# Kernel optimization log

Measured on AMD Instinct MI355X. Metric: run time of the kernel, lower is better.

Reference implementation:

```python
import jax, jax.numpy as jnp
import numpy as np

# dims
B = 4          # videos
F = 8          # frames (space_f)
P = 196        # patches per frame (time_n)
D = 768        # embed dim
H = 12         # heads
HD = D // H    # head dim
L = 4          # blocks
MLP = 4 * D
SCALE = HD ** -0.5
N = 1 + F * P  # sequence length with CLS


def setup_inputs() -> dict:
    key = jax.random.key(0)
    ks = jax.random.split(key, 20)
    s = 0.02
    w = lambda k, shape: (jax.random.normal(k, shape, jnp.float32) * s)
    inp = {
        'x': jax.random.normal(ks[0], (B, N, D), jnp.float32),
        # time attention params (stacked over layers); qkv_bias=False
        'qkv_w_t': w(ks[1], (L, 3 * D, D)),
        'proj_w_t': w(ks[2], (L, D, D)),
        'proj_b_t': jnp.zeros((L, D), jnp.float32),
        # space attention params
        'qkv_w_s': w(ks[3], (L, 3 * D, D)),
        'proj_w_s': w(ks[4], (L, D, D)),
        'proj_b_s': jnp.zeros((L, D), jnp.float32),
        # mlp
        'fc1_w': w(ks[5], (L, MLP, D)),
        'fc1_b': jnp.zeros((L, MLP), jnp.float32),
        'fc2_w': w(ks[6], (L, D, MLP)),
        'fc2_b': jnp.zeros((L, D), jnp.float32),
        # layernorms
        'ln1_g': jnp.ones((L, D), jnp.float32), 'ln1_b': jnp.zeros((L, D), jnp.float32),
        'ln2_g': jnp.ones((L, D), jnp.float32), 'ln2_b': jnp.zeros((L, D), jnp.float32),
        'ln3_g': jnp.ones((L, D), jnp.float32), 'ln3_b': jnp.zeros((L, D), jnp.float32),
    }
    return inp


def _ln(x, g, b):
    m = jnp.mean(x, axis=-1, keepdims=True)
    v = jnp.var(x, axis=-1, keepdims=True)
    return (x - m) * jax.lax.rsqrt(v + 1e-5) * g + b


def _attn(q, k, v):
    sim = jnp.einsum('bid,bjd->bij', q, k)
    a = jax.nn.softmax(sim, axis=-1)
    return jnp.einsum('bij,bjd->bid', a, v)


def _var_attn(x, qkv_w, proj_w, proj_b, mode):
    # x: [B, N, D]; mode in {'space','time'}
    qkv = x @ qkv_w.T                       # [B, N, 3D]
    q, k, v = jnp.split(qkv, 3, axis=-1)
    heads = lambda t: t.reshape(B, N, H, HD).transpose(0, 2, 1, 3).reshape(B * H, N, HD)
    q = heads(q) * SCALE
    k = heads(k)
    v = heads(v)
    cls_q, q_ = q[:, :1], q[:, 1:]
    cls_k, k_ = k[:, :1], k[:, 1:]
    cls_v, v_ = v[:, :1], v[:, 1:]
    # cls token attends over full sequence
    cls_out = _attn(cls_q, k, v)            # [(B h), 1, HD]
    BH = B * H
    if mode == 'space':
        # 'b (f n) d -> (b f) n d'
        split = lambda t: t.reshape(BH * F, P, HD)
        r, g, inner = F, F, P
    else:
        # 'b (f n) d -> (b n) f d'
        split = lambda t: t.reshape(BH, F, P, HD).transpose(0, 2, 1, 3).reshape(BH * P, F, HD)
        r, g, inner = P, P, F
    q_, k_, v_ = split(q_), split(k_), split(v_)
    # broadcast cls k/v across grouped batches: 'b () d -> (b r) () d'
    cls_k_r = jnp.repeat(cls_k, r, axis=0)
    cls_v_r = jnp.repeat(cls_v, r, axis=0)
    k_ = jnp.concatenate([cls_k_r, k_], axis=1)
    v_ = jnp.concatenate([cls_v_r, v_], axis=1)
    out = _attn(q_, k_, v_)                 # [(BH g), inner, HD]
    if mode == 'space':
        out = out.reshape(BH, F * P, HD)
    else:
        out = out.reshape(BH, P, F, HD).transpose(0, 2, 1, 3).reshape(BH, F * P, HD)
    out = jnp.concatenate([cls_out, out], axis=1)          # [(B h), N, HD]
    out = out.reshape(B, H, N, HD).transpose(0, 2, 1, 3).reshape(B, N, D)
    return out @ proj_w.T + proj_b


def _block(x, p):
    a = _ln(x, p['ln3_g'], p['ln3_b'])
    time_out = _var_attn(a, p['qkv_w_t'], p['proj_w_t'], p['proj_b_t'], 'time')
    time_residual = x + time_out
    space_out = _var_attn(_ln(time_residual, p['ln1_g'], p['ln1_b']),
                          p['qkv_w_s'], p['proj_w_s'], p['proj_b_s'], 'space')
    space_residual = x + space_out          # note: residual from original x (frozen-in-time style)
    h = _ln(space_residual, p['ln2_g'], p['ln2_b'])
    h = jax.nn.gelu(h @ p['fc1_w'].T + p['fc1_b'], approximate=False)
    h = h @ p['fc2_w'].T + p['fc2_b']
    return space_residual + h


def reference(x, qkv_w_t, proj_w_t, proj_b_t, qkv_w_s, proj_w_s, proj_b_s,
              fc1_w, fc1_b, fc2_w, fc2_b,
              ln1_g, ln1_b, ln2_g, ln2_b, ln3_g, ln3_b):
    params = dict(qkv_w_t=qkv_w_t, proj_w_t=proj_w_t, proj_b_t=proj_b_t,
                  qkv_w_s=qkv_w_s, proj_w_s=proj_w_s, proj_b_s=proj_b_s,
                  fc1_w=fc1_w, fc1_b=fc1_b, fc2_w=fc2_w, fc2_b=fc2_b,
                  ln1_g=ln1_g, ln1_b=ln1_b, ln2_g=ln2_g, ln2_b=ln2_b,
                  ln3_g=ln3_g, ln3_b=ln3_b)
    def step(carry, layer):
        return _block(carry, layer), None
    out, _ = jax.lax.scan(step, x, params)
    return out
```

## Files before the change

### kernel.cpp

```cpp
#include <hip/hip_runtime.h>
#include <cmath>

#define B_ 4
#define F_ 8
#define P_ 196
#define D_ 768
#define H_ 12
#define HD_ 64
#define L_ 4
#define MLP_ 3072
#define N_ (1 + F_*P_)
#define BN_ (B_*N_)
#define SCALE_ 0.125f
#define QKVC_ (3*D_)

typedef __bf16 bf16x8 __attribute__((ext_vector_type(8)));
typedef float f32x4 __attribute__((ext_vector_type(4)));
typedef const __attribute__((address_space(1))) void* gas_ptr;
typedef __attribute__((address_space(3))) void* las_ptr;

__device__ __forceinline__ unsigned short f2bf(float f) {
  union { __bf16 b; unsigned short u; } cv;
  cv.b = (__bf16)f;
  return cv.u;
}
__device__ __forceinline__ float bf2f(unsigned short u) {
  union { float f; unsigned int i; } cv; cv.i = ((unsigned int)u) << 16; return cv.f;
}
__device__ __forceinline__ unsigned int pk2(float a, float b) {
  return (unsigned int)f2bf(a) | ((unsigned int)f2bf(b) << 16);
}

__device__ __forceinline__ float gelu_exact(float x) {
  return 0.5f * x * (1.0f + erff(x * 0.70710678118654752f));
}

#define SQKV 1769472
#define SPROJ 589824
#define SFC 2359296

__device__ __forceinline__ void cvt_seg(const float* __restrict__ src,
                                        unsigned short* __restrict__ dst,
                                        int n, int t0, int stride) {
  for (int i = t0; i < (n >> 2); i += stride) {
    float4 v = ((const float4*)src)[i];
    ushort4 o;
    o.x = f2bf(v.x); o.y = f2bf(v.y); o.z = f2bf(v.z); o.w = f2bf(v.w);
    ((ushort4*)dst)[i] = o;
  }
}

__global__ __launch_bounds__(256) void cvt_layer_kernel(const float* qt, const float* pt,
                                                        const float* qs, const float* ps,
                                                        const float* f1, const float* f2,
                                                        unsigned short* wb) {
  int t0 = blockIdx.x * blockDim.x + threadIdx.x;
  int stride = gridDim.x * blockDim.x;
  cvt_seg(qt, wb + 0,       SQKV,  t0, stride);
  cvt_seg(pt, wb + 1769472, SPROJ, t0, stride);
  cvt_seg(qs, wb + 2359296, SQKV,  t0, stride);
  cvt_seg(ps, wb + 4128768, SPROJ, t0, stride);
  cvt_seg(f1, wb + 4718592, SFC,   t0, stride);
  cvt_seg(f2, wb + 7077888, SFC,   t0, stride);
}

__global__ __launch_bounds__(256) void ln_kernel(const float* __restrict__ x,
                                                 const float* __restrict__ g,
                                                 const float* __restrict__ b,
                                                 unsigned short* __restrict__ out) {
  int row = blockIdx.x;
  const float* xr = x + (size_t)row * D_;
  unsigned short* orow = out + (size_t)row * D_;
  int tid = threadIdx.x;
  float v0 = xr[tid], v1 = xr[tid + 256], v2 = xr[tid + 512];
  float s  = v0 + v1 + v2;
  float ss = v0*v0 + v1*v1 + v2*v2;
  #pragma unroll
  for (int o = 32; o > 0; o >>= 1) { s += __shfl_xor(s, o); ss += __shfl_xor(ss, o); }
  __shared__ float sm[8];
  int w = tid >> 6;
  if ((tid & 63) == 0) { sm[w*2] = s; sm[w*2+1] = ss; }
  __syncthreads();
  float tot  = sm[0] + sm[2] + sm[4] + sm[6];
  float tot2 = sm[1] + sm[3] + sm[5] + sm[7];
  float mean = tot * (1.0f/D_);
  float var  = tot2 * (1.0f/D_) - mean*mean;
  float rs   = rsqrtf(var + 1e-5f);
  orow[tid]       = f2bf((v0 - mean)*rs*g[tid]       + b[tid]);
  orow[tid + 256] = f2bf((v1 - mean)*rs*g[tid + 256] + b[tid + 256]);
  orow[tid + 512] = f2bf((v2 - mean)*rs*g[tid + 512] + b[tid + 512]);
}

template<int EPI>
__global__ __launch_bounds__(256, 3) void mfma_gemmP(const unsigned short* __restrict__ A,
                                                     const unsigned short* __restrict__ W,
                                                     const float* __restrict__ bias,
                                                     const float* __restrict__ Res,
                                                     void* __restrict__ Cout,
                                                     int M, int NN, int K) {
  __shared__ __align__(16) unsigned short LdsRaw[2*3*128*32];
  unsigned short* LdsA = LdsRaw;
  unsigned short* LdsB = LdsRaw + 3*128*32;
  int tid = threadIdx.x;
  int w = tid >> 6, l = tid & 63;
  int fr = l & 15, fq = l >> 4;
  int wr = w >> 1, wc = w & 1;
  int gx = (M + 127) >> 7;
  int gy = (NN + 127) >> 7;

  int nwg = gridDim.x;
  int orig = blockIdx.x;
  int q8 = nwg >> 3, r8 = nwg & 7;
  int xcd = orig & 7, idx = orig >> 3;
  int wg = (xcd < r8 ? xcd*(q8+1) : r8*(q8+1) + (xcd-r8)*q8) + idx;
  const int GROUPM = 8;
  int npg = GROUPM * gy;
  int gid = wg / npg;
  int first_m = gid * GROUPM;
  int gsz = gx - first_m; if (gsz > GROUPM) gsz = GROUPM;
  int rem = wg - gid * npg;
  int pid_m = first_m + rem % gsz;
  int pid_n = rem / gsz;
  int m0 = pid_m * 128, n0 = pid_n * 128;

  const char* aSrc[2]; const char* bSrc[2];
  #pragma unroll
  for (int q = 0; q < 2; ++q) {
    int c = q*256 + tid;
    int row = c >> 2;
    int cb = ((c & 3) << 4) ^ (((row >> 1) & 3) << 4);
    int ra = m0 + row; if (ra >= M) ra = M - 1;
    aSrc[q] = (const char*)A + ((size_t)ra * K) * 2 + cb;
    bSrc[q] = (const char*)W + ((size_t)(n0 + row) * K) * 2 + cb;
  }

  f32x4 acc[4][4] = {};
  int nt = K >> 5;
  int lswz = ((fr >> 1) & 3) << 4;

#define STAGEP(buf, kt) do { int kb_ = (kt) * 64;                                                                      \
    __builtin_amdgcn_global_load_lds((gas_ptr)(aSrc[0]+kb_), (las_ptr)(&LdsA[(buf)*4096 + (0*256 + w*64)*8]), 16, 0, 0); \
    __builtin_amdgcn_global_load_lds((gas_ptr)(aSrc[1]+kb_), (las_ptr)(&LdsA[(buf)*4096 + (1*256 + w*64)*8]), 16, 0, 0); \
    __builtin_amdgcn_global_load_lds((gas_ptr)(bSrc[0]+kb_), (las_ptr)(&LdsB[(buf)*4096 + (0*256 + w*64)*8]), 16, 0, 0); \
    __builtin_amdgcn_global_load_lds((gas_ptr)(bSrc[1]+kb_), (las_ptr)(&LdsB[(buf)*4096 + (1*256 + w*64)*8]), 16, 0, 0); \
  } while (0)

  STAGEP(0, 0);
  STAGEP(1, 1);
  int cur = 0;
  for (int t = 0; t < nt; ++t) {
    if (t + 1 < nt) {
      asm volatile("s_waitcnt vmcnt(4)" ::: "memory");
    } else {
      asm volatile("s_waitcnt vmcnt(0)" ::: "memory");
    }
    __builtin_amdgcn_s_barrier();
    const char* bufA = (const char*)(LdsA + cur*4096);
    const char* bufB = (const char*)(LdsB + cur*4096);
    bf16x8 afrag[4], bfrag[4];
    #pragma unroll
    for (int n = 0; n < 4; ++n)
      bfrag[n] = *(const bf16x8*)(bufB + (wc*64 + n*16 + fr)*64 + ((fq*16) ^ lswz));
    #pragma unroll
    for (int m = 0; m < 4; ++m)
      afrag[m] = *(const bf16x8*)(bufA + (wr*64 + m*16 + fr)*64 + ((fq*16) ^ lswz));
    #pragma unroll
    for (int m = 0; m < 4; ++m)
      #pragma unroll
      for (int n = 0; n < 4; ++n)
        acc[m][n] = __builtin_amdgcn_mfma_f32_16x16x32_bf16(afrag[m], bfrag[n], acc[m][n], 0, 0, 0);
    if (t + 2 < nt) {
      int nb = cur + 2; if (nb >= 3) nb -= 3;
      STAGEP(nb, t + 2);
    }
    ++cur; if (cur == 3) cur = 0;
  }
#undef STAGEP

  float* eps = (float*)LdsRaw;
  #pragma unroll
  for (int h = 0; h < 2; ++h) {
    __syncthreads();
    if (wr == h) {
      #pragma unroll
      for (int n = 0; n < 4; ++n)
        #pragma unroll
        for (int i = 0; i < 4; ++i)
          #pragma unroll
          for (int r = 0; r < 4; ++r) {
            int lrow = i*16 + fq*4 + r;
            int col  = wc*64 + n*16 + fr;
            eps[lrow*128 + (col ^ (((lrow >> 2) & 7) << 2))] = acc[i][n][r];
          }
    }
    __syncthreads();
    #pragma unroll
    for (int p = 0; p < 8; ++p) {
      int idx = p*256 + tid;
      int lrow = idx >> 5, cg = idx & 31;
      int col0 = cg * 4;
      int grow = m0 + h*64 + lrow;
      if (grow < M) {
        f32x4 v = *(const f32x4*)&eps[lrow*128 + (col0 ^ (((lrow >> 2) & 7) << 2))];
        int gcol = n0 + col0;
        if (EPI == 1 || EPI == 2) {
          float4 bv = *(const float4*)&bias[gcol];
          v[0] += bv.x; v[1] += bv.y; v[2] += bv.z; v[3] += bv.w;
        }
        if (EPI == 1) {
          float4 rv = *(const float4*)&Res[(size_t)grow * NN + gcol];
          v[0] += rv.x; v[1] += rv.y; v[2] += rv.z; v[3] += rv.w;
          *(float4*)&((float*)Cout)[(size_t)grow * NN + gcol] = make_float4(v[0], v[1], v[2], v[3]);
        } else if (EPI == 0) {
          *(float4*)&((float*)Cout)[(size_t)grow * NN + gcol] = make_float4(v[0], v[1], v[2], v[3]);
        } else {
          if (EPI == 2) {
            v[0] = gelu_exact(v[0]); v[1] = gelu_exact(v[1]);
            v[2] = gelu_exact(v[2]); v[3] = gelu_exact(v[3]);
          }
          unsigned long long ov = (unsigned long long)pk2(v[0], v[1])
                                | ((unsigned long long)pk2(v[2], v[3]) << 32);
          *(unsigned long long*)&((unsigned short*)Cout)[(size_t)grow * NN + gcol] = ov;
        }
      }
    }
  }
}

template<int EPI>
__global__ __launch_bounds__(256, 2) void mfma_gemmW(const unsigned short* __restrict__ A,
                                                     const unsigned short* __restrict__ W,
                                                     const float* __restrict__ bias,
                                                     const float* __restrict__ Res,
                                                     void* __restrict__ Cout,
                                                     int M, int NN, int K) {
  __shared__ __align__(16) unsigned short LdsRaw[3*256*32 + 3*128*32];
  unsigned short* LdsA = LdsRaw;
  unsigned short* LdsB = LdsRaw + 3*256*32;
  int tid = threadIdx.x;
  int w = tid >> 6, l = tid & 63;
  int fr = l & 15, fq = l >> 4;
  int wr = w >> 1, wc = w & 1;
  int gx = (M + 255) >> 8;
  int gy = (NN + 127) >> 7;

  int nwg = gridDim.x;
  int orig = blockIdx.x;
  int q8 = nwg >> 3, r8 = nwg & 7;
  int xcd = orig & 7, idx = orig >> 3;
  int wg = (xcd < r8 ? xcd*(q8+1) : r8*(q8+1) + (xcd-r8)*q8) + idx;
  const int GROUPM = 4;
  int npg = GROUPM * gy;
  int gid = wg / npg;
  int first_m = gid * GROUPM;
  int gsz = gx - first_m; if (gsz > GROUPM) gsz = GROUPM;
  int rem = wg - gid * npg;
  int pid_m = first_m + rem % gsz;
  int pid_n = rem / gsz;
  int m0 = pid_m * 256, n0 = pid_n * 128;

  const char* aSrc[4]; const char* bSrc[2];
  #pragma unroll
  for (int q = 0; q < 4; ++q) {
    int c = q*256 + tid;
    int row = c >> 2;
    int cb = ((c & 3) << 4) ^ (((row >> 1) & 3) << 4);
    int ra = m0 + row; if (ra >= M) ra = M - 1;
    aSrc[q] = (const char*)A + ((size_t)ra * K) * 2 + cb;
  }
  #pragma unroll
  for (int q = 0; q < 2; ++q) {
    int c = q*256 + tid;
    int row = c >> 2;
    int cb = ((c & 3) << 4) ^ (((row >> 1) & 3) << 4);
    bSrc[q] = (const char*)W + ((size_t)(n0 + row) * K) * 2 + cb;
  }

  f32x4 acc[8][4] = {};
  int nt = K >> 5;
  int lswz = ((fr >> 1) & 3) << 4;

#define STAGEW(buf, kt) do { int kb_ = (kt) * 64;                                                                      \
    __builtin_amdgcn_global_load_lds((gas_ptr)(aSrc[0]+kb_), (las_ptr)(&LdsA[(buf)*8192 + (0*256 + w*64)*8]), 16, 0, 0); \
    __builtin_amdgcn_global_load_lds((gas_ptr)(aSrc[1]+kb_), (las_ptr)(&LdsA[(buf)*8192 + (1*256 + w*64)*8]), 16, 0, 0); \
    __builtin_amdgcn_global_load_lds((gas_ptr)(aSrc[2]+kb_), (las_ptr)(&LdsA[(buf)*8192 + (2*256 + w*64)*8]), 16, 0, 0); \
    __builtin_amdgcn_global_load_lds((gas_ptr)(aSrc[3]+kb_), (las_ptr)(&LdsA[(buf)*8192 + (3*256 + w*64)*8]), 16, 0, 0); \
    __builtin_amdgcn_global_load_lds((gas_ptr)(bSrc[0]+kb_), (las_ptr)(&LdsB[(buf)*4096 + (0*256 + w*64)*8]), 16, 0, 0); \
    __builtin_amdgcn_global_load_lds((gas_ptr)(bSrc[1]+kb_), (las_ptr)(&LdsB[(buf)*4096 + (1*256 + w*64)*8]), 16, 0, 0); \
  } while (0)

  STAGEW(0, 0);
  STAGEW(1, 1);
  int cur = 0;
  for (int t = 0; t < nt; ++t) {
    if (t + 1 < nt) {
      asm volatile("s_waitcnt vmcnt(6)" ::: "memory");
    } else {
      asm volatile("s_waitcnt vmcnt(0)" ::: "memory");
    }
    __builtin_amdgcn_s_barrier();
    const char* bufA = (const char*)(LdsA + cur*8192);
    const char* bufB = (const char*)(LdsB + cur*4096);
    bf16x8 afrag[8], bfrag[4];
    #pragma unroll
    for (int n = 0; n < 4; ++n)
      bfrag[n] = *(const bf16x8*)(bufB + (wc*64 + n*16 + fr)*64 + ((fq*16) ^ lswz));
    #pragma unroll
    for (int m = 0; m < 8; ++m)
      afrag[m] = *(const bf16x8*)(bufA + (wr*128 + m*16 + fr)*64 + ((fq*16) ^ lswz));
    #pragma unroll
    for (int m = 0; m < 8; ++m)
      #pragma unroll
      for (int n = 0; n < 4; ++n)
        acc[m][n] = __builtin_amdgcn_mfma_f32_16x16x32_bf16(afrag[m], bfrag[n], acc[m][n], 0, 0, 0);
    if (t + 2 < nt) {
      int nb = cur + 2; if (nb >= 3) nb -= 3;
      STAGEW(nb, t + 2);
    }
    ++cur; if (cur == 3) cur = 0;
  }
#undef STAGEW

  float* eps = (float*)LdsRaw;
  #pragma unroll
  for (int qh = 0; qh < 4; ++qh) {
    __syncthreads();
    if (wr == (qh >> 1)) {
      int mbase = (qh & 1) * 4;
      #pragma unroll
      for (int n = 0; n < 4; ++n)
        #pragma unroll
        for (int mi = 0; mi < 4; ++mi)
          #pragma unroll
          for (int r = 0; r < 4; ++r) {
            int lrow = mi*16 + fq*4 + r;
            int col  = wc*64 + n*16 + fr;
            eps[lrow*128 + (col ^ (((lrow >> 2) & 7) << 2))] = acc[mbase + mi][n][r];
          }
    }
    __syncthreads();
    #pragma unroll
    for (int p = 0; p < 8; ++p) {
      int idx = p*256 + tid;
      int lrow = idx >> 5, cg = idx & 31;
      int col0 = cg * 4;
      int grow = m0 + qh*64 + lrow;
      if (grow < M) {
        f32x4 v = *(const f32x4*)&eps[lrow*128 + (col0 ^ (((lrow >> 2) & 7) << 2))];
        int gcol = n0 + col0;
        if (EPI == 1 || EPI == 2) {
          float4 bv = *(const float4*)&bias[gcol];
          v[0] += bv.x; v[1] += bv.y; v[2] += bv.z; v[3] += bv.w;
        }
        if (EPI == 1) {
          float4 rv = *(const float4*)&Res[(size_t)grow * NN + gcol];
          v[0] += rv.x; v[1] += rv.y; v[2] += rv.z; v[3] += rv.w;
          *(float4*)&((float*)Cout)[(size_t)grow * NN + gcol] = make_float4(v[0], v[1], v[2], v[3]);
        } else if (EPI == 0) {
          *(float4*)&((float*)Cout)[(size_t)grow * NN + gcol] = make_float4(v[0], v[1], v[2], v[3]);
        } else {
          if (EPI == 2) {
            v[0] = gelu_exact(v[0]); v[1] = gelu_exact(v[1]);
            v[2] = gelu_exact(v[2]); v[3] = gelu_exact(v[3]);
          }
          unsigned long long ov = (unsigned long long)pk2(v[0], v[1])
                                | ((unsigned long long)pk2(v[2], v[3]) << 32);
          *(unsigned long long*)&((unsigned short*)Cout)[(size_t)grow * NN + gcol] = ov;
        }
      }
    }
  }
}

#define CLS_CH 7
#define CLS_CHSZ 256
__global__ __launch_bounds__(256) void cls_attn_part(const unsigned short* __restrict__ qkv,
                                                     float* __restrict__ part) {
  int blk = blockIdx.x;
  int c = blk % CLS_CH, bh = blk / CLS_CH;
  int b = bh / H_, h = bh % H_;
  const unsigned short* base = qkv + (size_t)b * N_ * QKVC_ + h * HD_;
  __shared__ float q[HD_];
  __shared__ float s[CLS_CHSZ];
  __shared__ float redm[4], redd[4];
  __shared__ float pvs[4][HD_];
  int tid = threadIdx.x;
  if (tid < HD_) q[tid] = bf2f(base[tid]) * SCALE_;
  __syncthreads();
  int j = c * CLS_CHSZ + tid;
  float sc = -1e30f;
  if (j < N_) {
    const unsigned short* kp = base + (size_t)j * QKVC_ + D_;
    float acc = 0.f;
    #pragma unroll
    for (int cc = 0; cc < 8; ++cc) {
      uint4 kv = *(const uint4*)(kp + cc*8);
      const unsigned short* e = (const unsigned short*)&kv;
      #pragma unroll
      for (int t = 0; t < 8; ++t) acc = fmaf(q[cc*8+t], bf2f(e[t]), acc);
    }
    sc = acc;
  }
  float m = sc;
  #pragma unroll
  for (int o = 32; o > 0; o >>= 1) m = fmaxf(m, __shfl_xor(m, o));
  if ((tid & 63) == 0) redm[tid >> 6] = m;
  __syncthreads();
  m = fmaxf(fmaxf(redm[0], redm[1]), fmaxf(redm[2], redm[3]));
  float p = (j < N_) ? __expf(sc - m) : 0.f;
  s[tid] = p;
  float den = p;
  #pragma unroll
  for (int o = 32; o > 0; o >>= 1) den += __shfl_xor(den, o);
  if ((tid & 63) == 0) redd[tid >> 6] = den;
  __syncthreads();
  float dtot = redd[0] + redd[1] + redd[2] + redd[3];
  int lane = tid & 63, g = tid >> 6;
  float acc = 0.f;
  #pragma unroll 8
  for (int i = 0; i < CLS_CHSZ/4; ++i) {
    int jl = g + 4*i;
    int jj = c * CLS_CHSZ + jl;
    if (jj < N_) acc = fmaf(s[jl], bf2f(base[(size_t)jj * QKVC_ + 2*D_ + lane]), acc);
  }
  pvs[g][lane] = acc;
  __syncthreads();
  if (g == 0) {
    float pv = pvs[0][lane] + pvs[1][lane] + pvs[2][lane] + pvs[3][lane];
    float* pp = part + ((size_t)bh * CLS_CH + c) * 66;
    if (lane == 0) { pp[0] = m; pp[1] = dtot; }
    pp[2 + lane] = pv;
  }
}

__global__ __launch_bounds__(64) void cls_attn_reduce(const float* __restrict__ part,
                                                      unsigned short* __restrict__ att) {
  int bh = blockIdx.x;
  int b = bh / H_, h = bh % H_;
  int lane = threadIdx.x;
  const float* pp = part + (size_t)bh * CLS_CH * 66;
  float m = -1e30f;
  #pragma unroll
  for (int c = 0; c < CLS_CH; ++c) m = fmaxf(m, pp[c*66]);
  float den = 0.f, acc = 0.f;
  #pragma unroll
  for (int c = 0; c < CLS_CH; ++c) {
    float wfac = __expf(pp[c*66] - m);
    den += pp[c*66 + 1] * wfac;
    acc += pp[c*66 + 2 + lane] * wfac;
  }
  att[(size_t)(b * N_) * D_ + h * HD_ + lane] = f2bf(acc / den);
}

__global__ __launch_bounds__(256) void space_attn_mfma(const unsigned short* __restrict__ qkv,
                                                       unsigned short* __restrict__ att) {
  int blk = blockIdx.x;
  int f = blk % F_; int bh = blk / F_;
  int b = bh / H_, h = bh % H_;
  const unsigned short* qbase = qkv + (size_t)b * N_ * QKVC_ + h * HD_;
  __shared__ __align__(16) unsigned short Ksm[208*64];
  __shared__ __align__(16) unsigned short Vtm[64*256];
  __shared__ __align__(16) unsigned short Pm[4*16*256];
  int tid = threadIdx.x;

  for (int c = tid; c < 208*8; c += 256) {
    int j = c >> 3, cb = (c & 7) * 16;
    uint4 val = make_uint4(0,0,0,0);
    if (j < 197) {
      int n = (j == 0) ? 0 : (1 + f*P_ + j - 1);
      val = *(const uint4*)(qbase + (size_t)n*QKVC_ + D_ + cb/2);
    }
    *(uint4*)((char*)Ksm + j*128 + (cb ^ ((j&7)<<4))) = val;
  }
  for (int c = tid; c < 112*8; c += 256) {
    int jj = c % 112, dc = c / 112;
    int j0 = jj * 2;
    uint4 r0 = make_uint4(0,0,0,0), r1 = make_uint4(0,0,0,0);
    if (j0 < 197) {
      int n = (j0 == 0) ? 0 : (1 + f*P_ + j0 - 1);
      r0 = *(const uint4*)(qbase + (size_t)n*QKVC_ + 2*D_ + dc*8);
    }
    if (j0 + 1 < 197) {
      int n = 1 + f*P_ + j0;
      r1 = *(const uint4*)(qbase + (size_t)n*QKVC_ + 2*D_ + dc*8);
    }
    const unsigned short* e0 = (const unsigned short*)&r0;
    const unsigned short* e1 = (const unsigned short*)&r1;
    #pragma unroll
    for (int e = 0; e < 8; ++e) {
      int d = dc*8 + e;
      unsigned int pk = (unsigned int)e0[e] | ((unsigned int)e1[e] << 16);
      *(unsigned int*)((char*)Vtm + d*512 + ((2*j0) ^ ((d&7)<<4))) = pk;
    }
  }
  int w = tid >> 6, l = tid & 63;
  int fr = l & 15, fq = l >> 4;
  char* Pw = (char*)Pm + w * 8192;
  {
    int q = l >> 2, cb = 416 + (l & 3) * 8;
    *(unsigned long long*)(Pw + q*512 + (cb ^ ((q&7)<<4))) = 0ull;
  }
  __syncthreads();

  int swz = (fr & 7) << 4;
  for (int qt = w; qt <= 12; qt += 4) {
    int qrow = qt*16 + fr; if (qrow > 195) qrow = 195;
    int n_q = 1 + f*P_ + qrow;
    bf16x8 qf0 = *(const bf16x8*)(qbase + (size_t)n_q*QKVC_ + fq*8);
    bf16x8 qf1 = *(const bf16x8*)(qbase + (size_t)n_q*QKVC_ + 32 + fq*8);
    f32x4 s[13];
    #pragma unroll
    for (int jt = 0; jt < 13; ++jt) s[jt] = (f32x4){0.f,0.f,0.f,0.f};
    #pragma unroll
    for (int jt = 0; jt < 13; ++jt) {
      bf16x8 a0 = *(const bf16x8*)((char*)Ksm + (jt*16+fr)*128 + ((fq*16) ^ swz));
      s[jt] = __builtin_amdgcn_mfma_f32_16x16x32_bf16(a0, qf0, s[jt], 0, 0, 0);
      bf16x8 a1 = *(const bf16x8*)((char*)Ksm + (jt*16+fr)*128 + ((64 + fq*16) ^ swz));
      s[jt] = __builtin_amdgcn_mfma_f32_16x16x32_bf16(a1, qf1, s[jt], 0, 0, 0);
    }
    float m = -1e30f;
    #pragma unroll
    for (int jt = 0; jt < 13; ++jt) {
      #pragma unroll
      for (int r = 0; r < 4; ++r) {
        if (jt*16 + fq*4 + r < 197) m = fmaxf(m, s[jt][r]);
      }
    }
    m = fmaxf(m, __shfl_xor(m, 16));
    m = fmaxf(m, __shfl_xor(m, 32));
    float den = 0.f;
    #pragma unroll
    for (int jt = 0; jt < 13; ++jt) {
      #pragma unroll
      for (int r = 0; r < 4; ++r) {
        float p = (jt*16 + fq*4 + r < 197) ? __expf((s[jt][r] - m) * SCALE_) : 0.f;
        s[jt][r] = p;
        den += p;
      }
    }
    den += __shfl_xor(den, 16);
    den += __shfl_xor(den, 32);
    #pragma unroll
    for (int jt = 0; jt < 13; ++jt) {
      unsigned long long pv = (unsigned long long)pk2(s[jt][0], s[jt][1])
                            | ((unsigned long long)pk2(s[jt][2], s[jt][3]) << 32);
      *(unsigned long long*)(Pw + fr*512 + ((jt*32 + fq*8) ^ swz)) = pv;
    }
    float rden = 1.0f / den;
    bool wr_ok = (qt*16 + fr) < 196;
    int n_out = 1 + f*P_ + qt*16 + fr;
    #pragma unroll
    for (int dt = 0; dt < 4; ++dt) {
      f32x4 o = (f32x4){0.f,0.f,0.f,0.f};
      #pragma unroll
      for (int ks = 0; ks < 7; ++ks) {
        bf16x8 av = *(const bf16x8*)((char*)Vtm + (dt*16+fr)*512 + ((ks*64 + fq*16) ^ swz));
        bf16x8 bp = *(const bf16x8*)(Pw + fr*512 + ((ks*64 + fq*16) ^ swz));
        o = __builtin_amdgcn_mfma_f32_16x16x32_bf16(av, bp, o, 0, 0, 0);
      }
      if (wr_ok) {
        unsigned long long ov = (unsigned long long)pk2(o[0]*rden, o[1]*rden)
                              | ((unsigned long long)pk2(o[2]*rden, o[3]*rden) << 32);
        *(unsigned long long*)(att + (size_t)(b*N_ + n_out)*D_ + h*HD_ + dt*16 + fq*4) = ov;
      }
    }
  }
}

__global__ __launch_bounds__(256) void time_attn_kernel(const unsigned short* __restrict__ qkv,
                                                        unsigned short* __restrict__ att) {
  int idx = blockIdx.x * 4 + (threadIdx.x >> 6);
  int bh = idx / P_, p = idx % P_;
  int b = bh / H_, h = bh % H_;
  int lane = threadIdx.x & 63;
  const unsigned short* base = qkv + (size_t)b * N_ * QKVC_ + h * HD_ + lane;
  float k[9], v[9];
  k[0] = bf2f(base[D_]);
  v[0] = bf2f(base[2*D_]);
  #pragma unroll
  for (int j = 0; j < 8; ++j) {
    size_t r = (size_t)(1 + j * P_ + p) * QKVC_;
    k[j+1] = bf2f(base[r + D_]);
    v[j+1] = bf2f(base[r + 2*D_]);
  }
  #pragma unroll 1
  for (int f = 0; f < F_; ++f) {
    size_t qr = (size_t)(1 + f * P_ + p) * QKVC_;
    float qd = bf2f(base[qr]) * SCALE_;
    float s[9];
    #pragma unroll
    for (int j = 0; j < 9; ++j) {
      float prod = qd * k[j];
      #pragma unroll
      for (int o = 32; o > 0; o >>= 1) prod += __shfl_xor(prod, o);
      s[j] = prod;
    }
    float m = s[0];
    #pragma unroll
    for (int j = 1; j < 9; ++j) m = fmaxf(m, s[j]);
    float den = 0.f, o_ = 0.f;
    #pragma unroll
    for (int j = 0; j < 9; ++j) {
      float pj = __expf(s[j] - m);
      den += pj;
      o_ = fmaf(pj, v[j], o_);
    }
    att[(size_t)(b * N_ + 1 + f * P_ + p) * D_ + h * HD_ + lane] = f2bf(o_ / den);
  }
}

extern "C" void kernel_launch(void* const* d_in, const int* in_sizes, int n_in,
                              void* d_out, int out_size, void* d_ws, size_t ws_size,
                              hipStream_t stream) {
  const float* x_in     = (const float*)d_in[0];
  const float* qkv_w_t  = (const float*)d_in[1];
  const float* proj_w_t = (const float*)d_in[2];
  const float* proj_b_t = (const float*)d_in[3];
  const float* qkv_w_s  = (const float*)d_in[4];
  const float* proj_w_s = (const float*)d_in[5];
  const float* proj_b_s = (const float*)d_in[6];
  const float* fc1_w    = (const float*)d_in[7];
  const float* fc1_b    = (const float*)d_in[8];
  const float* fc2_w    = (const float*)d_in[9];
  const float* fc2_b    = (const float*)d_in[10];
  const float* ln1_g    = (const float*)d_in[11];
  const float* ln1_b    = (const float*)d_in[12];
  const float* ln2_g    = (const float*)d_in[13];
  const float* ln2_b    = (const float*)d_in[14];
  const float* ln3_g    = (const float*)d_in[15];
  const float* ln3_b    = (const float*)d_in[16];

  float* X_out = (float*)d_out;
  char* ws = (char*)d_ws;
  unsigned short* Wbf = (unsigned short*)ws;
  const size_t WOFF = 18874368;
  unsigned short* QKVbf = (unsigned short*)(ws + WOFF);
  unsigned short* Hbf   = (unsigned short*)(ws + WOFF);
  float*          TR    = (float*)(ws + WOFF + 57839616);
  unsigned short* Abf   = (unsigned short*)(ws + WOFF + 57839616 + 19279872);
  float*          CLSP  = (float*)(ws + WOFF + 57839616 + 19279872 + 9639936);

  unsigned short* wqkv_t = Wbf + 0;
  unsigned short* wproj_t= Wbf + 1769472;
  unsigned short* wqkv_s = Wbf + 2359296;
  unsigned short* wproj_s= Wbf + 4128768;
  unsigned short* wfc1   = Wbf + 4718592;
  unsigned short* wfc2   = Wbf + 7077888;

  dim3 blk(256);
  dim3 g_qkv(25 * 18), g_fc1(25 * 24);
  dim3 g_proj(50 * 6), g_fc2(50 * 6);

  for (int l = 0; l < L_; ++l) {
    const float* X = (l == 0) ? x_in : (const float*)X_out;
    cvt_layer_kernel<<<2048, blk, 0, stream>>>(
        qkv_w_t + (size_t)l*SQKV, proj_w_t + (size_t)l*SPROJ,
        qkv_w_s + (size_t)l*SQKV, proj_w_s + (size_t)l*SPROJ,
        fc1_w + (size_t)l*SFC, fc2_w + (size_t)l*SFC, Wbf);
    ln_kernel<<<BN_, blk, 0, stream>>>(X, ln3_g + l*D_, ln3_b + l*D_, Abf);
    mfma_gemmW<3><<<g_qkv, blk, 0, stream>>>(Abf, wqkv_t, nullptr, nullptr, QKVbf, BN_, QKVC_, D_);
    cls_attn_part<<<B_*H_*CLS_CH, blk, 0, stream>>>(QKVbf, CLSP);
    cls_attn_reduce<<<B_*H_, dim3(64), 0, stream>>>(CLSP, Abf);
    time_attn_kernel<<<(B_*H_*P_)/4, blk, 0, stream>>>(QKVbf, Abf);
    mfma_gemmP<1><<<g_proj, blk, 0, stream>>>(Abf, wproj_t, proj_b_t + l*D_, X, TR, BN_, D_, D_);
    ln_kernel<<<BN_, blk, 0, stream>>>(TR, ln1_g + l*D_, ln1_b + l*D_, Abf);
    mfma_gemmW<3><<<g_qkv, blk, 0, stream>>>(Abf, wqkv_s, nullptr, nullptr, QKVbf, BN_, QKVC_, D_);
    cls_attn_part<<<B_*H_*CLS_CH, blk, 0, stream>>>(QKVbf, CLSP);
    cls_attn_reduce<<<B_*H_, dim3(64), 0, stream>>>(CLSP, Abf);
    space_attn_mfma<<<B_*H_*F_, blk, 0, stream>>>(QKVbf, Abf);
    mfma_gemmP<1><<<g_proj, blk, 0, stream>>>(Abf, wproj_s, proj_b_s + l*D_, X, TR, BN_, D_, D_);
    ln_kernel<<<BN_, blk, 0, stream>>>(TR, ln2_g + l*D_, ln2_b + l*D_, Abf);
    mfma_gemmW<2><<<g_fc1, blk, 0, stream>>>(Abf, wfc1, fc1_b + l*MLP_, nullptr, Hbf, BN_, MLP_, D_);
    mfma_gemmP<1><<<g_fc2, blk, 0, stream>>>(Hbf, wfc2, fc2_b + l*D_, TR, X_out, BN_, D_, MLP_);
  }
}
```

Measured before the change: 1.832 ms.

## Shrink GEMM tiles, switch to double-buffered LDS, and retile N=768 GEMMs

The GEMM kernels move from triple-buffered LDS to double buffering, with an explicit LDS-read fence and barrier before the next stage overwrites the current buffer. The wide 256x128 kernel becomes a 128x64 kernel used for the N=768 projection and fc2 GEMMs, while QKV and fc1 now use the 128x128 kernel with occupancy raised to 4 blocks. The aim is higher occupancy and more workgroups on the smaller GEMMs, at the cost of less data reuse per tile, an extra barrier per k-step, and a shallower prefetch pipeline.

```diff
diff --git a/kernel.cpp b/kernel.cpp
--- a/kernel.cpp
+++ b/kernel.cpp
@@ -34,6 +34,11 @@
 __device__ __forceinline__ float gelu_exact(float x) {
   return 0.5f * x * (1.0f + erff(x * 0.70710678118654752f));
 }
+
+#define LDS_READ_FENCE() do {                                  \
+    asm volatile("s_waitcnt lgkmcnt(0)" ::: "memory");         \
+    __builtin_amdgcn_sched_barrier(0);                         \
+  } while (0)
 
 #define SQKV 1769472
 #define SPROJ 589824
@@ -92,15 +97,15 @@
 }
 
 template<int EPI>
-__global__ __launch_bounds__(256, 3) void mfma_gemmP(const unsigned short* __restrict__ A,
+__global__ __launch_bounds__(256, 4) void mfma_gemmP(const unsigned short* __restrict__ A,
                                                      const unsigned short* __restrict__ W,
                                                      const float* __restrict__ bias,
                                                      const float* __restrict__ Res,
                                                      void* __restrict__ Cout,
                                                      int M, int NN, int K) {
-  __shared__ __align__(16) unsigned short LdsRaw[2*3*128*32];
+  __shared__ __align__(16) unsigned short LdsRaw[2*2*128*32];
   unsigned short* LdsA = LdsRaw;
-  unsigned short* LdsB = LdsRaw + 3*128*32;
+  unsigned short* LdsB = LdsRaw + 2*128*32;
   int tid = threadIdx.x;
   int w = tid >> 6, l = tid & 63;
   int fr = l & 15, fq = l >> 4;
@@ -169,11 +174,12 @@
       #pragma unroll
       for (int n = 0; n < 4; ++n)
         acc[m][n] = __builtin_amdgcn_mfma_f32_16x16x32_bf16(afrag[m], bfrag[n], acc[m][n], 0, 0, 0);
+    LDS_READ_FENCE();
+    __builtin_amdgcn_s_barrier();
     if (t + 2 < nt) {
-      int nb = cur + 2; if (nb >= 3) nb -= 3;
-      STAGEP(nb, t + 2);
-    }
-    ++cur; if (cur == 3) cur = 0;
+      STAGEP(cur, t + 2);
+    }
+    cur ^= 1;
   }
 #undef STAGEP
 
@@ -228,28 +234,28 @@
 }
 
 template<int EPI>
-__global__ __launch_bounds__(256, 2) void mfma_gemmW(const unsigned short* __restrict__ A,
+__global__ __launch_bounds__(256, 4) void mfma_gemmN(const unsigned short* __restrict__ A,
                                                      const unsigned short* __restrict__ W,
                                                      const float* __restrict__ bias,
                                                      const float* __restrict__ Res,
                                                      void* __restrict__ Cout,
                                                      int M, int NN, int K) {
-  __shared__ __align__(16) unsigned short LdsRaw[3*256*32 + 3*128*32];
+  __shared__ __align__(16) unsigned short LdsRaw[2*128*32 + 2*64*32];
   unsigned short* LdsA = LdsRaw;
-  unsigned short* LdsB = LdsRaw + 3*256*32;
+  unsigned short* LdsB = LdsRaw + 2*128*32;
   int tid = threadIdx.x;
   int w = tid >> 6, l = tid & 63;
   int fr = l & 15, fq = l >> 4;
   int wr = w >> 1, wc = w & 1;
-  int gx = (M + 255) >> 8;
-  int gy = (NN + 127) >> 7;
+  int gx = (M + 127) >> 7;
+  int gy = (NN + 63) >> 6;
 
   int nwg = gridDim.x;
   int orig = blockIdx.x;
   int q8 = nwg >> 3, r8 = nwg & 7;
   int xcd = orig & 7, idx = orig >> 3;
   int wg = (xcd < r8 ? xcd*(q8+1) : r8*(q8+1) + (xcd-r8)*q8) + idx;
-  const int GROUPM = 4;
+  const int GROUPM = 8;
   int npg = GROUPM * gy;
   int gid = wg / npg;
   int first_m = gid * GROUPM;
@@ -257,96 +263,92 @@
   int rem = wg - gid * npg;
   int pid_m = first_m + rem % gsz;
   int pid_n = rem / gsz;
-  int m0 = pid_m * 256, n0 = pid_n * 128;
-
-  const char* aSrc[4]; const char* bSrc[2];
-  #pragma unroll
-  for (int q = 0; q < 4; ++q) {
+  int m0 = pid_m * 128, n0 = pid_n * 64;
+
+  const char* aSrc[2]; const char* bSrc;
+  #pragma unroll
+  for (int q = 0; q < 2; ++q) {
     int c = q*256 + tid;
     int row = c >> 2;
     int cb = ((c & 3) << 4) ^ (((row >> 1) & 3) << 4);
     int ra = m0 + row; if (ra >= M) ra = M - 1;
     aSrc[q] = (const char*)A + ((size_t)ra * K) * 2 + cb;
   }
-  #pragma unroll
-  for (int q = 0; q < 2; ++q) {
-    int c = q*256 + tid;
+  {
+    int c = tid;
     int row = c >> 2;
     int cb = ((c & 3) << 4) ^ (((row >> 1) & 3) << 4);
-    bSrc[q] = (const char*)W + ((size_t)(n0 + row) * K) * 2 + cb;
-  }
-
-  f32x4 acc[8][4] = {};
+    bSrc = (const char*)W + ((size_t)(n0 + row) * K) * 2 + cb;
+  }
+
+  f32x4 acc[4][2] = {};
   int nt = K >> 5;
   int lswz = ((fr >> 1) & 3) << 4;
 
-#define STAGEW(buf, kt) do { int kb_ = (kt) * 64;                                                                      \
-    __builtin_amdgcn_global_load_lds((gas_ptr)(aSrc[0]+kb_), (las_ptr)(&LdsA[(buf)*8192 + (0*256 + w*64)*8]), 16, 0, 0); \
-    __builtin_amdgcn_global_load_lds((gas_ptr)(aSrc[1]+kb_), (las_ptr)(&LdsA[(buf)*8192 + (1*256 + w*64)*8]), 16, 0, 0); \
-    __builtin_amdgcn_global_load_lds((gas_ptr)(aSrc[2]+kb_), (las_ptr)(&LdsA[(buf)*8192 + (2*256 + w*64)*8]), 16, 0, 0); \
-    __builtin_amdgcn_global_load_lds((gas_ptr)(aSrc[3]+kb_), (las_ptr)(&LdsA[(buf)*8192 + (3*256 + w*64)*8]), 16, 0, 0); \
-    __builtin_amdgcn_global_load_lds((gas_ptr)(bSrc[0]+kb_), (las_ptr)(&LdsB[(buf)*4096 + (0*256 + w*64)*8]), 16, 0, 0); \
-    __builtin_amdgcn_global_load_lds((gas_ptr)(bSrc[1]+kb_), (las_ptr)(&LdsB[(buf)*4096 + (1*256 + w*64)*8]), 16, 0, 0); \
+#define STAGEN(buf, kt) do { int kb_ = (kt) * 64;                                                                      \
+    __builtin_amdgcn_global_load_lds((gas_ptr)(aSrc[0]+kb_), (las_ptr)(&LdsA[(buf)*4096 + (0*256 + w*64)*8]), 16, 0, 0); \
+    __builtin_amdgcn_global_load_lds((gas_ptr)(aSrc[1]+kb_), (las_ptr)(&LdsA[(buf)*4096 + (1*256 + w*64)*8]), 16, 0, 0); \
+    __builtin_amdgcn_global_load_lds((gas_ptr)(bSrc+kb_),    (las_ptr)(&LdsB[(buf)*2048 + (w*64)*8]),         16, 0, 0); \
   } while (0)
 
-  STAGEW(0, 0);
-  STAGEW(1, 1);
+  STAGEN(0, 0);
+  STAGEN(1, 1);
   int cur = 0;
   for (int t = 0; t < nt; ++t) {
     if (t + 1 < nt) {
-      asm volatile("s_waitcnt vmcnt(6)" ::: "memory");
+      asm volatile("s_waitcnt vmcnt(3)" ::: "memory");
     } else {
       asm volatile("s_waitcnt vmcnt(0)" ::: "memory");
     }
     __builtin_amdgcn_s_barrier();
-    const char* bufA = (const char*)(LdsA + cur*8192);
-    const char* bufB = (const char*)(LdsB + cur*4096);
-    bf16x8 afrag[8], bfrag[4];
-    #pragma unroll
-    for (int n = 0; n < 4; ++n)
-      bfrag[n] = *(const bf16x8*)(bufB + (wc*64 + n*16 + fr)*64 + ((fq*16) ^ lswz));
-    #pragma unroll
-    for (int m = 0; m < 8; ++m)
-      afrag[m] = *(const bf16x8*)(bufA + (wr*128 + m*16 + fr)*64 + ((fq*16) ^ lswz));
-    #pragma unroll
-    for (int m = 0; m < 8; ++m)
-      #pragma unroll
-      for (int n = 0; n < 4; ++n)
+    const char* bufA = (const char*)(LdsA + cur*4096);
+    const char* bufB = (const char*)(LdsB + cur*2048);
+    bf16x8 afrag[4], bfrag[2];
+    #pragma unroll
+    for (int n = 0; n < 2; ++n)
+      bfrag[n] = *(const bf16x8*)(bufB + (wc*32 + n*16 + fr)*64 + ((fq*16) ^ lswz));
+    #pragma unroll
+    for (int m = 0; m < 4; ++m)
+      afrag[m] = *(const bf16x8*)(bufA + (wr*64 + m*16 + fr)*64 + ((fq*16) ^ lswz));
+    #pragma unroll
+    for (int m = 0; m < 4; ++m)
+      #pragma unroll
+      for (int n = 0; n < 2; ++n)
         acc[m][n] = __builtin_amdgcn_mfma_f32_16x16x32_bf16(afrag[m], bfrag[n], acc[m][n], 0, 0, 0);
+    LDS_READ_FENCE();
+    __builtin_amdgcn_s_barrier();
     if (t + 2 < nt) {
-      int nb = cur + 2; if (nb >= 3) nb -= 3;
-      STAGEW(nb, t + 2);
-    }
-    ++cur; if (cur == 3) cur = 0;
-  }
-#undef STAGEW
+      STAGEN(cur, t + 2);
+    }
+    cur ^= 1;
+  }
+#undef STAGEN
 
   float* eps = (float*)LdsRaw;
   #pragma unroll
-  for (int qh = 0; qh < 4; ++qh) {
+  for (int h = 0; h < 2; ++h) {
     __syncthreads();
-    if (wr == (qh >> 1)) {
-      int mbase = (qh & 1) * 4;
-      #pragma unroll
-      for (int n = 0; n < 4; ++n)
+    if (wr == h) {
+      #pragma unroll
+      for (int n = 0; n < 2; ++n)
         #pragma unroll
-        for (int mi = 0; mi < 4; ++mi)
+        for (int i = 0; i < 4; ++i)
           #pragma unroll
           for (int r = 0; r < 4; ++r) {
-            int lrow = mi*16 + fq*4 + r;
-            int col  = wc*64 + n*16 + fr;
-            eps[lrow*128 + (col ^ (((lrow >> 2) & 7) << 2))] = acc[mbase + mi][n][r];
+            int lrow = i*16 + fq*4 + r;
+            int col  = wc*32 + n*16 + fr;
+            eps[lrow*64 + (col ^ (((lrow >> 2) & 7) << 2))] = acc[i][n][r];
           }
     }
     __syncthreads();
     #pragma unroll
-    for (int p = 0; p < 8; ++p) {
+    for (int p = 0; p < 4; ++p) {
       int idx = p*256 + tid;
-      int lrow = idx >> 5, cg = idx & 31;
+      int lrow = idx >> 4, cg = idx & 15;
       int col0 = cg * 4;
-      int grow = m0 + qh*64 + lrow;
+      int grow = m0 + h*64 + lrow;
       if (grow < M) {
-        f32x4 v = *(const f32x4*)&eps[lrow*128 + (col0 ^ (((lrow >> 2) & 7) << 2))];
+        f32x4 v = *(const f32x4*)&eps[lrow*64 + (col0 ^ (((lrow >> 2) & 7) << 2))];
         int gcol = n0 + col0;
         if (EPI == 1 || EPI == 2) {
           float4 bv = *(const float4*)&bias[gcol];
@@ -648,8 +650,8 @@
   unsigned short* wfc2   = Wbf + 7077888;
 
   dim3 blk(256);
-  dim3 g_qkv(25 * 18), g_fc1(25 * 24);
-  dim3 g_proj(50 * 6), g_fc2(50 * 6);
+  dim3 g_qkv(50 * 18), g_fc1(50 * 24);
+  dim3 g_n768(50 * 12);
 
   for (int l = 0; l < L_; ++l) {
     const float* X = (l == 0) ? x_in : (const float*)X_out;
@@ -658,19 +660,19 @@
         qkv_w_s + (size_t)l*SQKV, proj_w_s + (size_t)l*SPROJ,
         fc1_w + (size_t)l*SFC, fc2_w + (size_t)l*SFC, Wbf);
     ln_kernel<<<BN_, blk, 0, stream>>>(X, ln3_g + l*D_, ln3_b + l*D_, Abf);
-    mfma_gemmW<3><<<g_qkv, blk, 0, stream>>>(Abf, wqkv_t, nullptr, nullptr, QKVbf, BN_, QKVC_, D_);
+    mfma_gemmP<3><<<g_qkv, blk, 0, stream>>>(Abf, wqkv_t, nullptr, nullptr, QKVbf, BN_, QKVC_, D_);
     cls_attn_part<<<B_*H_*CLS_CH, blk, 0, stream>>>(QKVbf, CLSP);
     cls_attn_reduce<<<B_*H_, dim3(64), 0, stream>>>(CLSP, Abf);
     time_attn_kernel<<<(B_*H_*P_)/4, blk, 0, stream>>>(QKVbf, Abf);
-    mfma_gemmP<1><<<g_proj, blk, 0, stream>>>(Abf, wproj_t, proj_b_t + l*D_, X, TR, BN_, D_, D_);
+    mfma_gemmN<1><<<g_n768, blk, 0, stream>>>(Abf, wproj_t, proj_b_t + l*D_, X, TR, BN_, D_, D_);
     ln_kernel<<<BN_, blk, 0, stream>>>(TR, ln1_g + l*D_, ln1_b + l*D_, Abf);
-    mfma_gemmW<3><<<g_qkv, blk, 0, stream>>>(Abf, wqkv_s, nullptr, nullptr, QKVbf, BN_, QKVC_, D_);
+    mfma_gemmP<3><<<g_qkv, blk, 0, stream>>>(Abf, wqkv_s, nullptr, nullptr, QKVbf, BN_, QKVC_, D_);
     cls_attn_part<<<B_*H_*CLS_CH, blk, 0, stream>>>(QKVbf, CLSP);
     cls_attn_reduce<<<B_*H_, dim3(64), 0, stream>>>(CLSP, Abf);
     space_attn_mfma<<<B_*H_*F_, blk, 0, stream>>>(QKVbf, Abf);
-    mfma_gemmP<1><<<g_proj, blk, 0, stream>>>(Abf, wproj_s, proj_b_s + l*D_, X, TR, BN_, D_, D_);
+    mfma_gemmN<1><<<g_n768, blk, 0, stream>>>(Abf, wproj_s, proj_b_s + l*D_, X, TR, BN_, D_, D_);
     ln_kernel<<<BN_, blk, 0, stream>>>(TR, ln2_g + l*D_, ln2_b + l*D_, Abf);
-    mfma_gemmW<2><<<g_fc1, blk, 0, stream>>>(Abf, wfc1, fc1_b + l*MLP_, nullptr, Hbf, BN_, MLP_, D_);
-    mfma_gemmP<1><<<g_fc2, blk, 0, stream>>>(Hbf, wfc2, fc2_b + l*D_, TR, X_out, BN_, D_, MLP_);
-  }
-}
+    mfma_gemmP<2><<<g_fc1, blk, 0, stream>>>(Abf, wfc1, fc1_b + l*MLP_, nullptr, Hbf, BN_, MLP_, D_);
+    mfma_gemmN<1><<<g_n768, blk, 0, stream>>>(Hbf, wfc2, fc2_b + l*D_, TR, X_out, BN_, D_, MLP_);
+  }
+}
```

New measurement: 1.588 ms. -13.3%, faster.
